# Performance work log

Hardware: AMD Instinct MI355X
Metric: run time of the kernel (lower is better)

The kernel has to match this reference:

```python
import jax, jax.numpy as jnp
import numpy as np

NEG = -1000000.0

def setup_inputs() -> dict:
    key = jax.random.key(0)
    ks = jax.random.split(key, 7)
    B, Q, K, H, Dv = 8, 512, 512, 64, 64
    queries = jax.random.normal(ks[0], (B, Q, H), dtype=jnp.float32)
    keys = jax.random.normal(ks[1], (B, K, H), dtype=jnp.float32)
    values = jax.random.normal(ks[2], (B, K, Dv), dtype=jnp.float32)
    valid_lens = jax.random.randint(ks[3], (B,), 1, K + 1)
    # learned params (torch Linear without bias); stored as [in, out]
    Wq = jax.random.normal(ks[4], (H, H), dtype=jnp.float32) / np.sqrt(H)
    Wk = jax.random.normal(ks[5], (H, H), dtype=jnp.float32) / np.sqrt(H)
    wv = jax.random.normal(ks[6], (H,), dtype=jnp.float32) / np.sqrt(H)
    return {"queries": queries, "keys": keys, "values": values,
            "valid_lens": valid_lens, "Wq": Wq, "Wk": Wk, "wv": wv}

def reference(queries, keys, values, valid_lens, Wq, Wk, wv):
    q = queries @ Wq                      # [B,Q,H]
    k = keys @ Wk                         # [B,K,H]
    # broadcast-add -> tanh -> rank-1 score projection
    feat = jnp.tanh(q[:, :, None, :] + k[:, None, :, :])   # [B,Q,K,H]
    scores = jnp.einsum('bqkh,h->bqk', feat, wv)            # [B,Q,K]
    # masked softmax over key axis: positions >= valid_len get -1e6
    Klen = scores.shape[-1]
    mask = jnp.arange(Klen)[None, None, :] < valid_lens[:, None, None]
    scores = jnp.where(mask, scores, NEG)
    attn = jax.nn.softmax(scores, axis=-1)                  # [B,Q,K]
    return jnp.einsum('bqk,bkd->bqd', attn, values)         # [B,Q,Dv]
```

## Files before the change

kernel.cpp:

```cpp
#include <hip/hip_runtime.h>

#define C2   2.8853900817779268f
#define NC2 -2.8853900817779268f

__global__ __launch_bounds__(256) void proj_exp_kernel(
    const float* __restrict__ queries,
    const float* __restrict__ keys,
    const float* __restrict__ Wq,
    const float* __restrict__ Wk,
    float* __restrict__ Eq,
    float* __restrict__ Ek)
{
    __shared__ float w_lds[64 * 64];
    __shared__ float in_lds[16 * 64];

    const int t   = threadIdx.x;
    const int blk = blockIdx.x;
    const int r0  = blk * 16;
    const bool isQ = (r0 < 4096);
    const float* __restrict__ W  = isQ ? Wq : Wk;
    const float* __restrict__ in = isQ ? queries : keys;
    float* __restrict__ Eo       = isQ ? Eq : Ek;
    const int rbase = isQ ? r0 : (r0 - 4096);

#pragma unroll
    for (int i = 0; i < 16; ++i)
        w_lds[t + i * 256] = W[t + i * 256];
#pragma unroll
    for (int i = 0; i < 4; ++i)
        in_lds[t + i * 256] = in[(size_t)rbase * 64 + t + i * 256];
    __syncthreads();

    const int h  = t & 63;
    const int rg = t >> 6;
    const float* inr = &in_lds[rg * 4 * 64];
    float acc0 = 0.f, acc1 = 0.f, acc2 = 0.f, acc3 = 0.f;
#pragma unroll
    for (int i = 0; i < 64; i += 4) {
        float4 r0_ = *reinterpret_cast<const float4*>(inr + 0 * 64 + i);
        float4 r1_ = *reinterpret_cast<const float4*>(inr + 1 * 64 + i);
        float4 r2_ = *reinterpret_cast<const float4*>(inr + 2 * 64 + i);
        float4 r3_ = *reinterpret_cast<const float4*>(inr + 3 * 64 + i);
        float w0 = w_lds[(i + 0) * 64 + h];
        float w1 = w_lds[(i + 1) * 64 + h];
        float w2 = w_lds[(i + 2) * 64 + h];
        float w3 = w_lds[(i + 3) * 64 + h];
        acc0 = fmaf(r0_.x, w0, acc0); acc0 = fmaf(r0_.y, w1, acc0);
        acc0 = fmaf(r0_.z, w2, acc0); acc0 = fmaf(r0_.w, w3, acc0);
        acc1 = fmaf(r1_.x, w0, acc1); acc1 = fmaf(r1_.y, w1, acc1);
        acc1 = fmaf(r1_.z, w2, acc1); acc1 = fmaf(r1_.w, w3, acc1);
        acc2 = fmaf(r2_.x, w0, acc2); acc2 = fmaf(r2_.y, w1, acc2);
        acc2 = fmaf(r2_.z, w2, acc2); acc2 = fmaf(r2_.w, w3, acc2);
        acc3 = fmaf(r3_.x, w0, acc3); acc3 = fmaf(r3_.y, w1, acc3);
        acc3 = fmaf(r3_.z, w2, acc3); acc3 = fmaf(r3_.w, w3, acc3);
    }
    float a[4] = {acc0, acc1, acc2, acc3};
#pragma unroll
    for (int j = 0; j < 4; ++j) {
        float x = fminf(fmaxf(a[j] * C2, -60.f), 60.f);
        Eo[(size_t)(rbase + rg * 4 + j) * 64 + h] = __builtin_amdgcn_exp2f(x);
    }
}

__global__ __launch_bounds__(512, 4) void attn_kernel(
    const float* __restrict__ Eq,
    const float* __restrict__ Ek,
    const float* __restrict__ wv,
    const float* __restrict__ V,
    const int* __restrict__ valid_lens,
    float* __restrict__ out)
{
    __shared__ float p_lds[8][512];
    __shared__ float part_lds[8 * 8 * 64];
    __shared__ float wv_lds[64];

    const int t   = threadIdx.x;
    const int bid = blockIdx.x;
    const int b   = bid >> 6;
    const int q0  = (bid & 63) << 3;
    const int l   = t & 63;
    const int w   = __builtin_amdgcn_readfirstlane(threadIdx.x >> 6);
    const int vl  = valid_lens[b];
    const int k   = w * 64 + l;
    const bool kvalid = (k < vl);
    const int nact = (vl + 63) >> 6;
    const bool wact = (w < nact);

    if (t < 64) wv_lds[t] = wv[t];

    const float* __restrict__ eqbase = Eq + (size_t)(b * 512 + q0) * 64;

    if (wact) {
        float ek[64];
        {
            const float4* ekr = reinterpret_cast<const float4*>(Ek + (size_t)(b * 512 + k) * 64);
#pragma unroll
            for (int i = 0; i < 16; ++i) {
                float4 v = ekr[i];
                ek[4 * i + 0] = v.x; ek[4 * i + 1] = v.y;
                ek[4 * i + 2] = v.z; ek[4 * i + 3] = v.w;
            }
        }
        __syncthreads();

#pragma unroll 1
        for (int q = 0; q < 8; ++q) {
            const float* __restrict__ eqp = eqbase + q * 64;
            float a0 = 0.f, a1 = 0.f, a2 = 0.f, a3 = 0.f;
#pragma unroll
            for (int h = 0; h < 64; h += 4) {
                float4 w4 = *reinterpret_cast<const float4*>(&wv_lds[h]);
                a0 = fmaf(w4.x, __builtin_amdgcn_rcpf(fmaf(eqp[h + 0], ek[h + 0], 1.f)), a0);
                a1 = fmaf(w4.y, __builtin_amdgcn_rcpf(fmaf(eqp[h + 1], ek[h + 1], 1.f)), a1);
                a2 = fmaf(w4.z, __builtin_amdgcn_rcpf(fmaf(eqp[h + 2], ek[h + 2], 1.f)), a2);
                a3 = fmaf(w4.w, __builtin_amdgcn_rcpf(fmaf(eqp[h + 3], ek[h + 3], 1.f)), a3);
            }
            float p = kvalid ? __builtin_amdgcn_exp2f(((a0 + a1) + (a2 + a3)) * NC2) : 0.f;
            p_lds[q][k] = p;
        }
    } else {
        __syncthreads();
#pragma unroll
        for (int q = 0; q < 8; ++q)
            p_lds[q][k] = 0.f;
    }

    float acc[8] = {0.f, 0.f, 0.f, 0.f, 0.f, 0.f, 0.f, 0.f};
    if (wact) {
        const float* __restrict__ Vb = V + (size_t)b * 512 * 64;
        const int kb = w * 64;
#pragma unroll 4
        for (int kk = 0; kk < 64; kk += 4) {
            const int k0 = kb + kk;
            float4 pq[8];
#pragma unroll
            for (int q = 0; q < 8; ++q)
                pq[q] = *reinterpret_cast<const float4*>(&p_lds[q][k0]);
            float v0 = Vb[(size_t)(k0 + 0) * 64 + l];
            float v1 = Vb[(size_t)(k0 + 1) * 64 + l];
            float v2 = Vb[(size_t)(k0 + 2) * 64 + l];
            float v3 = Vb[(size_t)(k0 + 3) * 64 + l];
#pragma unroll
            for (int q = 0; q < 8; ++q) {
                acc[q] = fmaf(pq[q].x, v0, acc[q]);
                acc[q] = fmaf(pq[q].y, v1, acc[q]);
                acc[q] = fmaf(pq[q].z, v2, acc[q]);
                acc[q] = fmaf(pq[q].w, v3, acc[q]);
            }
        }
    }
#pragma unroll
    for (int q = 0; q < 8; ++q)
        part_lds[(w * 8 + q) * 64 + l] = acc[q];
    __syncthreads();

    float dsum = 0.f;
#pragma unroll
    for (int j = 0; j < 8; ++j)
        dsum += p_lds[w][j * 64 + l];
#pragma unroll
    for (int off = 32; off > 0; off >>= 1)
        dsum += __shfl_xor(dsum, off);

    float o = 0.f;
#pragma unroll
    for (int ww = 0; ww < 8; ++ww)
        o += part_lds[(ww * 8 + w) * 64 + l];
    out[(size_t)(b * 512 + q0 + w) * 64 + l] = o * __builtin_amdgcn_rcpf(dsum);
}

extern "C" void kernel_launch(void* const* d_in, const int* in_sizes, int n_in,
                              void* d_out, int out_size, void* d_ws, size_t ws_size,
                              hipStream_t stream) {
    (void)in_sizes; (void)n_in; (void)out_size; (void)ws_size;
    const float* queries = (const float*)d_in[0];
    const float* keys    = (const float*)d_in[1];
    const float* values  = (const float*)d_in[2];
    const int*   vlens   = (const int*)d_in[3];
    const float* Wq      = (const float*)d_in[4];
    const float* Wk      = (const float*)d_in[5];
    const float* wv      = (const float*)d_in[6];
    float* out = (float*)d_out;

    float* Eq = (float*)d_ws;
    float* Ek = Eq + 8 * 512 * 64;

    proj_exp_kernel<<<512, 256, 0, stream>>>(queries, keys, Wq, Wk, Eq, Ek);
    attn_kernel<<<512, 512, 0, stream>>>(Eq, Ek, wv, values, vlens, out);
}
```

Baseline: 43.46 us.

## Split attention over two key chunks with a separate combine kernel

```diff
diff --git a/kernel.cpp b/kernel.cpp
--- a/kernel.cpp
+++ b/kernel.cpp
@@ -62,33 +62,44 @@
     }
 }
 
-__global__ __launch_bounds__(512, 4) void attn_kernel(
+__global__ __launch_bounds__(256, 4) void attn_kernel(
     const float* __restrict__ Eq,
     const float* __restrict__ Ek,
     const float* __restrict__ wv,
     const float* __restrict__ V,
     const int* __restrict__ valid_lens,
-    float* __restrict__ out)
+    float* __restrict__ Opart,
+    float* __restrict__ Dpart)
 {
-    __shared__ float p_lds[8][512];
-    __shared__ float part_lds[8 * 8 * 64];
+    __shared__ float p_lds[8][256];
+    __shared__ float part_lds[4][8][64];
+    __shared__ float eq_lds[512];
     __shared__ float wv_lds[64];
 
     const int t   = threadIdx.x;
     const int bid = blockIdx.x;
-    const int b   = bid >> 6;
-    const int q0  = (bid & 63) << 3;
+    const int kc  = bid >> 9;
+    const int rem = bid & 511;
+    const int b   = rem >> 6;
+    const int qt  = rem & 63;
+    const int q0  = qt << 3;
     const int l   = t & 63;
     const int w   = __builtin_amdgcn_readfirstlane(threadIdx.x >> 6);
     const int vl  = valid_lens[b];
-    const int k   = w * 64 + l;
+    const int kl  = w * 64 + l;
+    const int k   = kc * 256 + kl;
     const bool kvalid = (k < vl);
-    const int nact = (vl + 63) >> 6;
-    const bool wact = (w < nact);
-
-    if (t < 64) wv_lds[t] = wv[t];
-
-    const float* __restrict__ eqbase = Eq + (size_t)(b * 512 + q0) * 64;
+    const bool wact   = (kc * 256 + w * 64) < vl;
+
+    {
+        const float* eqg = Eq + (size_t)(b * 512 + q0) * 64;
+        eq_lds[t]       = eqg[t];
+        eq_lds[t + 256] = eqg[t + 256];
+        if (t < 64) wv_lds[t] = wv[t];
+    }
+    __syncthreads();
+
+    float acc[8] = {0.f, 0.f, 0.f, 0.f, 0.f, 0.f, 0.f, 0.f};
 
     if (wact) {
         float ek[64];
@@ -101,45 +112,43 @@
                 ek[4 * i + 2] = v.z; ek[4 * i + 3] = v.w;
             }
         }
-        __syncthreads();
 
 #pragma unroll 1
         for (int q = 0; q < 8; ++q) {
-            const float* __restrict__ eqp = eqbase + q * 64;
+            const float* eql = &eq_lds[q * 64];
             float a0 = 0.f, a1 = 0.f, a2 = 0.f, a3 = 0.f;
 #pragma unroll
-            for (int h = 0; h < 64; h += 4) {
-                float4 w4 = *reinterpret_cast<const float4*>(&wv_lds[h]);
-                a0 = fmaf(w4.x, __builtin_amdgcn_rcpf(fmaf(eqp[h + 0], ek[h + 0], 1.f)), a0);
-                a1 = fmaf(w4.y, __builtin_amdgcn_rcpf(fmaf(eqp[h + 1], ek[h + 1], 1.f)), a1);
-                a2 = fmaf(w4.z, __builtin_amdgcn_rcpf(fmaf(eqp[h + 2], ek[h + 2], 1.f)), a2);
-                a3 = fmaf(w4.w, __builtin_amdgcn_rcpf(fmaf(eqp[h + 3], ek[h + 3], 1.f)), a3);
+            for (int h = 0; h < 64; h += 8) {
+                float4 e0 = *reinterpret_cast<const float4*>(eql + h);
+                float4 e1 = *reinterpret_cast<const float4*>(eql + h + 4);
+                float4 w0 = *reinterpret_cast<const float4*>(wv_lds + h);
+                float4 w1 = *reinterpret_cast<const float4*>(wv_lds + h + 4);
+                a0 = fmaf(w0.x, __builtin_amdgcn_rcpf(fmaf(e0.x, ek[h + 0], 1.f)), a0);
+                a1 = fmaf(w0.y, __builtin_amdgcn_rcpf(fmaf(e0.y, ek[h + 1], 1.f)), a1);
+                a2 = fmaf(w0.z, __builtin_amdgcn_rcpf(fmaf(e0.z, ek[h + 2], 1.f)), a2);
+                a3 = fmaf(w0.w, __builtin_amdgcn_rcpf(fmaf(e0.w, ek[h + 3], 1.f)), a3);
+                a0 = fmaf(w1.x, __builtin_amdgcn_rcpf(fmaf(e1.x, ek[h + 4], 1.f)), a0);
+                a1 = fmaf(w1.y, __builtin_amdgcn_rcpf(fmaf(e1.y, ek[h + 5], 1.f)), a1);
+                a2 = fmaf(w1.z, __builtin_amdgcn_rcpf(fmaf(e1.z, ek[h + 6], 1.f)), a2);
+                a3 = fmaf(w1.w, __builtin_amdgcn_rcpf(fmaf(e1.w, ek[h + 7], 1.f)), a3);
             }
             float p = kvalid ? __builtin_amdgcn_exp2f(((a0 + a1) + (a2 + a3)) * NC2) : 0.f;
-            p_lds[q][k] = p;
+            p_lds[q][kl] = p;
         }
-    } else {
-        __syncthreads();
-#pragma unroll
-        for (int q = 0; q < 8; ++q)
-            p_lds[q][k] = 0.f;
-    }
-
-    float acc[8] = {0.f, 0.f, 0.f, 0.f, 0.f, 0.f, 0.f, 0.f};
-    if (wact) {
+
         const float* __restrict__ Vb = V + (size_t)b * 512 * 64;
-        const int kb = w * 64;
+        const int kb = kc * 256 + w * 64;
+        const int kbl = w * 64;
 #pragma unroll 4
         for (int kk = 0; kk < 64; kk += 4) {
-            const int k0 = kb + kk;
             float4 pq[8];
 #pragma unroll
             for (int q = 0; q < 8; ++q)
-                pq[q] = *reinterpret_cast<const float4*>(&p_lds[q][k0]);
-            float v0 = Vb[(size_t)(k0 + 0) * 64 + l];
-            float v1 = Vb[(size_t)(k0 + 1) * 64 + l];
-            float v2 = Vb[(size_t)(k0 + 2) * 64 + l];
-            float v3 = Vb[(size_t)(k0 + 3) * 64 + l];
+                pq[q] = *reinterpret_cast<const float4*>(&p_lds[q][kbl + kk]);
+            float v0 = Vb[(size_t)(kb + kk + 0) * 64 + l];
+            float v1 = Vb[(size_t)(kb + kk + 1) * 64 + l];
+            float v2 = Vb[(size_t)(kb + kk + 2) * 64 + l];
+            float v3 = Vb[(size_t)(kb + kk + 3) * 64 + l];
 #pragma unroll
             for (int q = 0; q < 8; ++q) {
                 acc[q] = fmaf(pq[q].x, v0, acc[q]);
@@ -148,25 +157,49 @@
                 acc[q] = fmaf(pq[q].w, v3, acc[q]);
             }
         }
-    }
+    } else {
+#pragma unroll
+        for (int q = 0; q < 8; ++q)
+            p_lds[q][kl] = 0.f;
+    }
+
 #pragma unroll
     for (int q = 0; q < 8; ++q)
-        part_lds[(w * 8 + q) * 64 + l] = acc[q];
+        part_lds[w][q][l] = acc[q];
     __syncthreads();
 
-    float dsum = 0.f;
-#pragma unroll
-    for (int j = 0; j < 8; ++j)
-        dsum += p_lds[w][j * 64 + l];
-#pragma unroll
-    for (int off = 32; off > 0; off >>= 1)
-        dsum += __shfl_xor(dsum, off);
-
-    float o = 0.f;
-#pragma unroll
-    for (int ww = 0; ww < 8; ++ww)
-        o += part_lds[(ww * 8 + w) * 64 + l];
-    out[(size_t)(b * 512 + q0 + w) * 64 + l] = o * __builtin_amdgcn_rcpf(dsum);
+    const size_t tile = (size_t)(kc * 512 + rem);
+#pragma unroll
+    for (int j = 0; j < 2; ++j) {
+        const int q = w * 2 + j;
+        float ds = p_lds[q][l] + p_lds[q][l + 64] + p_lds[q][l + 128] + p_lds[q][l + 192];
+#pragma unroll
+        for (int off = 32; off > 0; off >>= 1)
+            ds += __shfl_xor(ds, off);
+        float o = part_lds[0][q][l] + part_lds[1][q][l]
+                + part_lds[2][q][l] + part_lds[3][q][l];
+        Opart[(tile * 8 + q) * 64 + l] = o;
+        if (l == 0) Dpart[tile * 8 + q] = ds;
+    }
+}
+
+__global__ __launch_bounds__(256) void combine_kernel(
+    const float* __restrict__ Opart,
+    const float* __restrict__ Dpart,
+    float* __restrict__ out)
+{
+    const int bid = blockIdx.x;
+    const int t   = threadIdx.x;
+    const int l   = t & 63;
+#pragma unroll
+    for (int j = 0; j < 2; ++j) {
+        const int q = (t >> 6) + j * 4;
+        const size_t i0 = ((size_t)(0 * 512 + bid) * 8 + q) * 64 + l;
+        const size_t i1 = ((size_t)(1 * 512 + bid) * 8 + q) * 64 + l;
+        float o   = Opart[i0] + Opart[i1];
+        float den = Dpart[(0 * 512 + bid) * 8 + q] + Dpart[(1 * 512 + bid) * 8 + q];
+        out[((size_t)bid * 8 + q) * 64 + l] = o * __builtin_amdgcn_rcpf(den);
+    }
 }
 
 extern "C" void kernel_launch(void* const* d_in, const int* in_sizes, int n_in,
@@ -182,9 +215,12 @@
     const float* wv      = (const float*)d_in[6];
     float* out = (float*)d_out;
 
-    float* Eq = (float*)d_ws;
-    float* Ek = Eq + 8 * 512 * 64;
+    float* Eq    = (float*)d_ws;
+    float* Ek    = Eq + 262144;
+    float* Opart = Ek + 262144;
+    float* Dpart = Opart + 524288;
 
     proj_exp_kernel<<<512, 256, 0, stream>>>(queries, keys, Wq, Wk, Eq, Ek);
-    attn_kernel<<<512, 512, 0, stream>>>(Eq, Ek, wv, values, vlens, out);
-}
+    attn_kernel<<<1024, 256, 0, stream>>>(Eq, Ek, wv, values, vlens, Opart, Dpart);
+    combine_kernel<<<512, 256, 0, stream>>>(Opart, Dpart, out);
+}
```

Result: slower. 95.57 us (+119.9%).
